# Performance work log

Hardware: AMD Instinct MI355X
Metric: run time of the kernel (lower is better)

## Reference

```python
import jax, jax.numpy as jnp
import numpy as np

B = 32768
MARGIN = 0.1
P = 2.0          # norm_degree
EPS_BN = 1e-3    # BatchNorm1d eps=0.001
EPS_PD = 1e-6    # F.pairwise_distance eps


def setup_inputs() -> dict:
    key = jax.random.key(0)
    ks = jax.random.split(key, 40)
    W = lambda k, o, i: jax.random.normal(k, (o, i), jnp.float32) * 0.01
    inp = {
        'img_p': jax.random.normal(ks[0], (B, 300), jnp.float32),
        'img_n': jax.random.normal(ks[1], (B, 300), jnp.float32),
        'tag':   jax.random.normal(ks[2], (B, 300), jnp.float32),
        'lat':   jax.random.uniform(ks[3], (B, 1), jnp.float32),
        'lon':   jax.random.uniform(ks[4], (B, 1), jnp.float32),
        # fc_i_1 (Linear 300->1024 + BN)
        'Wi1': W(ks[5], 1024, 300), 'bi1': jnp.zeros(1024), 'gi1': jnp.ones(1024), 'bti1': jnp.zeros(1024),
        # fc_i_2, fc_i_3
        'Wi2': W(ks[6], 1024, 1024), 'bi2': jnp.zeros(1024),
        'Wi3': W(ks[7], 300, 1024), 'bi3': jnp.zeros(300),
        # fc_loc (Linear 2->10 + BN)
        'Wloc': W(ks[8], 10, 2), 'bloc': jnp.zeros(10), 'gloc': jnp.ones(10), 'btloc': jnp.zeros(10),
        # fc_mm_1..3 (Linear + BN), fc_mm_4
        'Wm1': W(ks[9], 1024, 310), 'bm1': jnp.zeros(1024), 'gm1': jnp.ones(1024), 'btm1': jnp.zeros(1024),
        'Wm2': W(ks[10], 1024, 1024), 'bm2': jnp.zeros(1024), 'gm2': jnp.ones(1024), 'btm2': jnp.zeros(1024),
        'Wm3': W(ks[11], 1024, 1024), 'bm3': jnp.zeros(1024), 'gm3': jnp.ones(1024), 'btm3': jnp.zeros(1024),
        'Wm4': W(ks[12], 300, 1024), 'bm4': jnp.zeros(300),
    }
    return inp


def _fc_bn_relu(x, W, b, g, beta):
    # Linear -> BatchNorm1d (training mode, biased batch stats) -> ReLU
    y = x @ W.T + b
    m = jnp.mean(y, axis=0)
    v = jnp.mean((y - m) ** 2, axis=0)
    return jax.nn.relu((y - m) * jax.lax.rsqrt(v + EPS_BN) * g + beta)


def _pairwise_distance(x, y):
    # torch F.pairwise_distance with eps=1e-6
    return jnp.sum(jnp.abs(x - y + EPS_PD) ** P, axis=1) ** (1.0 / P)


def reference(img_p, img_n, tag, lat, lon,
              Wi1, bi1, gi1, bti1, Wi2, bi2, Wi3, bi3,
              Wloc, bloc, gloc, btloc,
              Wm1, bm1, gm1, btm1, Wm2, bm2, gm2, btm2,
              Wm3, bm3, gm3, btm3, Wm4, bm4):
    def img_branch(x):
        x = _fc_bn_relu(x, Wi1, bi1, gi1, bti1)
        x = x @ Wi2.T + bi2
        x = x @ Wi3.T + bi3
        return x
    p = img_branch(img_p)   # [B, 300]
    n = img_branch(img_n)   # [B, 300] (separate BN batch stats, as in torch)
    loc = jnp.concatenate([lat, lon], axis=1)           # [B, 2]
    loc = _fc_bn_relu(loc, Wloc, bloc, gloc, btloc)     # [B, 10]
    a = jnp.concatenate([loc, tag], axis=1)             # [B, 310]
    a = _fc_bn_relu(a, Wm1, bm1, gm1, btm1)
    a = _fc_bn_relu(a, Wm2, bm2, gm2, btm2)
    a = _fc_bn_relu(a, Wm3, bm3, gm3, btm3)
    a = a @ Wm4.T + bm4                                 # [B, 300]
    d_tp = _pairwise_distance(a, p)
    d_tn = _pairwise_distance(a, n)
    # vectorized replacement for the per-element python count loop
    correct = jnp.sum(d_tn - d_tp > MARGIN).astype(jnp.int32).reshape(1)
    return (p, n, a, correct)
```

## Files before the change

### kernel.cpp

```cpp
#include <hip/hip_runtime.h>

typedef _Float16 f16;
typedef _Float16 half8 __attribute__((ext_vector_type(8)));
typedef float f32x4 __attribute__((ext_vector_type(4)));

__device__ __forceinline__ void gl_lds16(const void* g, void* l) {
  __builtin_amdgcn_global_load_lds(
      (__attribute__((address_space(1))) void*)(size_t)g,
      (__attribute__((address_space(3))) void*)l, 16, 0, 0);
}

template <int EPI, int BNA>
__global__ __launch_bounds__(512, 2) void gemm256_k(
    const f16* __restrict__ A, int Ksteps, int KP,
    void* __restrict__ outp, int ldOut, int Ncols,
    float2* __restrict__ partial, int r1, int kz, int oz,
    const f16* __restrict__ B0, const float* __restrict__ bias0,
    const f16* __restrict__ sc0, const f16* __restrict__ sh0,
    const f16* __restrict__ B1, const float* __restrict__ bias1,
    const f16* __restrict__ sc1, const f16* __restrict__ sh1) {
  __shared__ char smem[135168];

  const int t = threadIdx.x;
  const int lane = t & 63;
  const int wave = t >> 6;
  const int wm = wave >> 2, wn = wave & 3;
  const int l16 = lane & 15, lg = lane >> 4;

  int bx = blockIdx.x, by = blockIdx.y;
  {
    const int nwg = gridDim.x * gridDim.y;
    const int wg = bx + gridDim.x * by;
    const int cpx = nwg >> 3;
    const int newid = (wg & 7) * cpx + (wg >> 3);
    bx = newid % gridDim.x;
    by = newid / gridDim.x;
  }
  const int m0 = by * 256;
  const int n0 = bx * 256;

  const f16* Bw = (by >= r1) ? B1 : B0;
  const float* bias = (by >= r1) ? bias1 : bias0;
  const f16* scH = (by >= r1) ? sc1 : sc0;
  const f16* shH = (by >= r1) ? sh1 : sh0;

  f32x4 acc[8][4] = {};

  const int rA = t >> 2;
  const int g16 = ((t & 3) ^ ((t >> 3) & 3)) * 16;
  const f16* Ap = A + (size_t)(m0 >> 8) * 256 * KP + (size_t)blockIdx.z * kz;
  const f16* Bp = Bw + (size_t)(n0 >> 8) * 256 * KP + (size_t)blockIdx.z * kz;
  const char* gA = (const char*)Ap + rA * 64 + g16;
  const char* gB = (const char*)Bp + rA * 64 + g16;

  auto stage = [&](int slot, int kt) {
    const char* pA = gA + (size_t)kt * 16384;
    const char* pB = gB + (size_t)kt * 16384;
    char* d = smem + slot * 32768 + t * 16;
    gl_lds16(pA, d);
    gl_lds16(pA + 8192, d + 8192);
    gl_lds16(pB, d + 16384);
    gl_lds16(pB + 8192, d + 24576);
  };

  if constexpr (BNA) {
    if (t < 128)
      gl_lds16((const char*)scH + t * 16, smem + 131072 + t * 16);
    else if (t < 256)
      gl_lds16((const char*)shH + (t - 128) * 16, smem + 133120 + (t - 128) * 16);
  }
  stage(0, 0);
  stage(1, 1);
  stage(2, 2);
  asm volatile("s_waitcnt vmcnt(8)" ::: "memory");
  __builtin_amdgcn_s_barrier();
  asm volatile("" ::: "memory");

  const int xsw = (lg ^ ((l16 >> 1) & 3)) << 4;
  const int oA0 = (wm * 128 + l16) * 64 + xsw;
  const int oB0 = (wn * 64 + l16) * 64 + xsw;

  for (int kt = 0; kt < Ksteps; ++kt) {
    const char* bufA = smem + (kt & 3) * 32768;
    const char* bufB = bufA + 16384;
    half8 af[8], bf0, bf1, scv, shv;
#pragma unroll
    for (int m = 0; m < 8; ++m) af[m] = *(const half8*)(bufA + oA0 + m * 1024);
    bf0 = *(const half8*)(bufB + oB0);
    bf1 = *(const half8*)(bufB + oB0 + 1024);
    if constexpr (BNA) {
      scv = *(const half8*)(smem + 131072 + kt * 64 + lg * 16);
      shv = *(const half8*)(smem + 133120 + kt * 64 + lg * 16);
    }
    if (kt + 3 < Ksteps) {
      const char* pA = gA + (size_t)(kt + 3) * 16384;
      char* d = smem + ((kt + 3) & 3) * 32768 + t * 16;
      gl_lds16(pA, d);
      gl_lds16(pA + 8192, d + 8192);
    }
    asm volatile("" ::: "memory");
    __builtin_amdgcn_s_barrier();
    asm volatile("s_waitcnt lgkmcnt(0)" ::: "memory");
    if constexpr (BNA) {
      const half8 zeroh = {};
#pragma unroll
      for (int m = 0; m < 8; ++m)
        af[m] = __builtin_elementwise_max((half8)(af[m] * scv + shv), zeroh);
    }
    __builtin_amdgcn_s_setprio(1);
#pragma unroll
    for (int m = 0; m < 8; ++m) {
      acc[m][0] = __builtin_amdgcn_mfma_f32_16x16x32_f16(af[m], bf0, acc[m][0], 0, 0, 0);
      acc[m][1] = __builtin_amdgcn_mfma_f32_16x16x32_f16(af[m], bf1, acc[m][1], 0, 0, 0);
    }
    __builtin_amdgcn_s_setprio(0);
    half8 bf2 = *(const half8*)(bufB + oB0 + 2048);
    half8 bf3 = *(const half8*)(bufB + oB0 + 3072);
    if (kt + 3 < Ksteps) {
      const char* pB = gB + (size_t)(kt + 3) * 16384;
      char* d = smem + ((kt + 3) & 3) * 32768 + t * 16;
      gl_lds16(pB, d + 16384);
      gl_lds16(pB + 8192, d + 24576);
      asm volatile("s_waitcnt vmcnt(8)" ::: "memory");
    } else if (kt == Ksteps - 3) {
      asm volatile("s_waitcnt vmcnt(4)" ::: "memory");
    } else if (kt == Ksteps - 2) {
      asm volatile("s_waitcnt vmcnt(0)" ::: "memory");
    }
    asm volatile("" ::: "memory");
    __builtin_amdgcn_s_barrier();
    asm volatile("s_waitcnt lgkmcnt(0)" ::: "memory");
    __builtin_amdgcn_s_setprio(1);
#pragma unroll
    for (int m = 0; m < 8; ++m) {
      acc[m][2] = __builtin_amdgcn_mfma_f32_16x16x32_f16(af[m], bf2, acc[m][2], 0, 0, 0);
      acc[m][3] = __builtin_amdgcn_mfma_f32_16x16x32_f16(af[m], bf3, acc[m][3], 0, 0, 0);
    }
    __builtin_amdgcn_s_setprio(0);
  }

  __syncthreads();

  float* const swv = (float*)smem + wave * 1152;
  float biasv[4];
#pragma unroll
  for (int n = 0; n < 4; ++n) {
    const int c = n0 + wn * 64 + n * 16 + l16;
    biasv[n] = (bias != nullptr && c < Ncols) ? bias[c] : 0.f;
  }
  float cs[4] = {}, cq[4] = {};
  const int rowr = lane >> 2;
  const int colc = (lane & 3) << 4;

#pragma unroll
  for (int m = 0; m < 8; ++m) {
#pragma unroll
    for (int n = 0; n < 4; ++n)
#pragma unroll
      for (int r = 0; r < 4; ++r) {
        const float v = acc[m][n][r] + biasv[n];
        swv[(lg * 4 + r) * 68 + n * 16 + l16] = v;
        if constexpr (EPI == 0) {
          cs[n] += v;
          cq[n] += v * v;
        }
      }
    asm volatile("s_waitcnt lgkmcnt(0)" ::: "memory");
    const float* sp = swv + rowr * 68 + colc;
    const int grow = m0 + wm * 128 + m * 16 + rowr;
    if constexpr (EPI == 2) {
      float* rp = (float*)outp + (size_t)blockIdx.z * oz + (size_t)grow * ldOut;
#pragma unroll
      for (int j = 0; j < 4; ++j) {
        const int c = n0 + wn * 64 + colc + j * 4;
        const f32x4 v = *(const f32x4*)(sp + j * 4);
        if (c + 3 < Ncols) {
          *(f32x4*)(rp + c) = v;
        } else {
#pragma unroll
          for (int e = 0; e < 4; ++e)
            if (c + e < Ncols) rp[c + e] = v[e];
        }
      }
    } else {
      const f32x4 v0 = *(const f32x4*)(sp);
      const f32x4 v1 = *(const f32x4*)(sp + 4);
      const f32x4 v2 = *(const f32x4*)(sp + 8);
      const f32x4 v3 = *(const f32x4*)(sp + 12);
      half8 h0, h1;
#pragma unroll
      for (int e = 0; e < 4; ++e) {
        h0[e] = (f16)v0[e];
        h0[4 + e] = (f16)v1[e];
        h1[e] = (f16)v2[e];
        h1[4 + e] = (f16)v3[e];
      }
      f16* o16 = (f16*)outp;
      const size_t dstE = (size_t)(grow >> 8) * 262144 +
                          (size_t)((n0 >> 5) + wn * 2 + (colc >> 5)) * 8192 +
                          (size_t)(grow & 255) * 32 + (colc & 31);
      *(half8*)(o16 + dstE) = h0;
      *(half8*)(o16 + dstE + 8) = h1;
    }
    asm volatile("s_waitcnt lgkmcnt(0)" ::: "memory");
  }

  if constexpr (EPI == 0) {
    float2* pp = partial + ((size_t)(by * 2 + wm) * 4 + lg) * 1024 + n0 + wn * 64 + l16;
#pragma unroll
    for (int n = 0; n < 4; ++n) pp[n * 16] = make_float2(cs[n], cq[n]);
  }
}

__global__ void bn_red_k(const float2* __restrict__ partial, float2* __restrict__ part2) {
  const int c = blockIdx.x * 256 + threadIdx.x;
  const int chunk = blockIdx.y;
  const float2* p = partial + (size_t)chunk * 64 * 1024 + c;
  float s = 0.f, q = 0.f;
#pragma unroll 4
  for (int i = 0; i < 64; ++i) {
    float2 v = p[(size_t)i * 1024];
    s += v.x;
    q += v.y;
  }
  part2[(size_t)chunk * 1024 + c] = make_float2(s, q);
}

__global__ void bn_fin_k(const float2* __restrict__ part2, int chunkStart, int nchunks,
                         const float* __restrict__ g, const float* __restrict__ beta,
                         f16* __restrict__ scH, f16* __restrict__ shH, float invB) {
  const int c = blockIdx.x * 256 + threadIdx.x;
  float s = 0.f, q = 0.f;
  const float2* p = part2 + (size_t)chunkStart * 1024 + c;
  for (int i = 0; i < nchunks; ++i) {
    float2 v = p[(size_t)i * 1024];
    s += v.x;
    q += v.y;
  }
  float m = s * invB;
  float var = q * invB - m * m;
  float sc = rsqrtf(var + 1e-3f) * g[c];
  scH[c] = (f16)sc;
  shH[c] = (f16)(beta[c] - m * sc);
}

__global__ void bn_fin3_k(const float2* __restrict__ part2, int cps, float invB,
                          const float* __restrict__ g0, const float* __restrict__ b0,
                          f16* __restrict__ so0, f16* __restrict__ sh0,
                          const float* __restrict__ g1, const float* __restrict__ b1,
                          f16* __restrict__ so1, f16* __restrict__ sh1,
                          const float* __restrict__ g2, const float* __restrict__ b2,
                          f16* __restrict__ so2, f16* __restrict__ sh2) {
  const int j = blockIdx.y;
  const float* g = j == 0 ? g0 : (j == 1 ? g1 : g2);
  const float* bt = j == 0 ? b0 : (j == 1 ? b1 : b2);
  f16* so = j == 0 ? so0 : (j == 1 ? so1 : so2);
  f16* sh = j == 0 ? sh0 : (j == 1 ? sh1 : sh2);
  const int c = blockIdx.x * 256 + threadIdx.x;
  float s = 0.f, q = 0.f;
  const float2* p = part2 + (size_t)j * cps * 1024 + c;
  for (int i = 0; i < cps; ++i) {
    float2 v = p[(size_t)i * 1024];
    s += v.x;
    q += v.y;
  }
  float m = s * invB;
  float var = q * invB - m * m;
  float sc = rsqrtf(var + 1e-3f) * g[c];
  so[c] = (f16)sc;
  sh[c] = (f16)(bt[c] - m * sc);
}

__global__ void cvt_all_k(const float* __restrict__ Wi1, const float* __restrict__ Wm1,
                          const float* __restrict__ Wi3, const float* __restrict__ Wm2,
                          const float* __restrict__ Wm3, const float* __restrict__ Wm4,
                          f16* __restrict__ Wi1p, f16* __restrict__ Wm1p,
                          f16* __restrict__ Wi3p, f16* __restrict__ Wm2p,
                          f16* __restrict__ Wm3p, f16* __restrict__ Wm4p) {
  const int k = blockIdx.x * 256 + threadIdx.x;
  const int row = blockIdx.y;
  const float* src;
  f16* dst;
  int n, K, KP, Nreal;
  if (row < 2048) {
    KP = 384;
    if (row < 1024) { src = Wi1; dst = Wi1p; n = row; K = 300; Nreal = 1024; }
    else { src = Wm1; dst = Wm1p; n = row - 1024; K = 310; Nreal = 1024; }
  } else {
    KP = 1024;
    if (row < 2560) { src = Wi3; dst = Wi3p; n = row - 2048; K = 1024; Nreal = 300; }
    else if (row < 3584) { src = Wm2; dst = Wm2p; n = row - 2560; K = 1024; Nreal = 1024; }
    else if (row < 4608) { src = Wm3; dst = Wm3p; n = row - 3584; K = 1024; Nreal = 1024; }
    else { src = Wm4; dst = Wm4p; n = row - 4608; K = 1024; Nreal = 300; }
  }
  if (k >= KP) return;
  float v = (n < Nreal && k < K) ? src[(size_t)n * K + k] : 0.f;
  dst[(size_t)(n >> 8) * 256 * KP + (size_t)(k >> 5) * 8192 +
      (size_t)(n & 255) * 32 + (k & 31)] = (f16)v;
}

__global__ void cvt_wT_k(const float* __restrict__ W, f16* __restrict__ Wt) {
  __shared__ f16 tile[64][65];
  const int bx = blockIdx.x * 64, by = blockIdx.y * 64;
  const int tc = threadIdx.x & 63, tr = threadIdx.x >> 6;
#pragma unroll
  for (int r = tr; r < 64; r += 4)
    tile[r][tc] = (f16)W[(size_t)(by + r) * 1024 + bx + tc];
  __syncthreads();
#pragma unroll
  for (int r = tr; r < 64; r += 4) {
    const int nr = bx + r;
    const int kc = by + tc;
    Wt[(size_t)(nr >> 8) * 262144 + (size_t)(kc >> 5) * 8192 +
       (size_t)(nr & 255) * 32 + (kc & 31)] = tile[tc][r];
  }
}

__global__ void cvt_in_k(const float* __restrict__ ip, const float* __restrict__ in_,
                         const float* __restrict__ tg, f16* __restrict__ Ain, int B) {
  const int gid = blockIdx.x * 256 + threadIdx.x;
  const int row = gid / 48;
  const int c0 = (gid - row * 48) * 8;
  if (row >= B) return;
  half8 vp = {}, vn = {}, vm = {};
  const float* rp = ip + (size_t)row * 300;
  const float* rn = in_ + (size_t)row * 300;
  const float* rt = tg + (size_t)row * 300;
#pragma unroll
  for (int e = 0; e < 8; ++e) {
    const int c = c0 + e;
    if (c < 300) {
      vp[e] = (f16)rp[c];
      vn[e] = (f16)rn[c];
    }
    if (c >= 10 && c < 310) vm[e] = (f16)rt[c - 10];
  }
  const size_t o = (size_t)(row >> 8) * 98304 + (size_t)(c0 >> 5) * 8192 +
                   (size_t)(row & 255) * 32 + (c0 & 31);
  const size_t pstr = (size_t)(B >> 8) * 98304;
  *(half8*)(Ain + o) = vp;
  *(half8*)(Ain + pstr + o) = vn;
  *(half8*)(Ain + 2 * pstr + o) = vm;
}

__global__ void fold_red_k(const float* __restrict__ pf, f16* __restrict__ Wf) {
  const int i = blockIdx.x * 256 + threadIdx.x;
  float s = 0.f;
#pragma unroll
  for (int z = 0; z < 8; ++z) s += pf[(size_t)z * 524288 + i];
  const int n = i >> 10, k = i & 1023;
  Wf[(size_t)(n >> 8) * 262144 + (size_t)(k >> 5) * 8192 +
     (size_t)(n & 255) * 32 + (k & 31)] = (f16)s;
}

__global__ void bfold_k(const f16* __restrict__ Wi3p, const float* __restrict__ bi2,
                        const float* __restrict__ bi3, float* __restrict__ bf) {
  const int n = blockIdx.x;
  const int t = threadIdx.x;
  const size_t nb = (size_t)(n >> 8) * 262144 + (size_t)(n & 255) * 32;
  float s = 0.f;
  for (int j = t; j < 1024; j += 256)
    s += (float)Wi3p[nb + (size_t)(j >> 5) * 8192 + (j & 31)] * bi2[j];
#pragma unroll
  for (int off = 32; off; off >>= 1) s += __shfl_xor(s, off);
  __shared__ float red[4];
  if ((t & 63) == 0) red[t >> 6] = s;
  __syncthreads();
  if (t == 0) bf[n] = red[0] + red[1] + red[2] + red[3] + (n < 300 ? bi3[n] : 0.f);
}

__global__ void loc_stats_k(const float* __restrict__ lat, const float* __restrict__ lon,
                            const float* __restrict__ Wloc, const float* __restrict__ bloc,
                            float* __restrict__ partial) {
  const int t = threadIdx.x;
  const int row = blockIdx.x * 256 + t;
  float la = lat[row], lo = lon[row];
  float s[10], q[10];
#pragma unroll
  for (int j = 0; j < 10; ++j) {
    float y = la * Wloc[j * 2] + lo * Wloc[j * 2 + 1] + bloc[j];
    s[j] = y;
    q[j] = y * y;
  }
#pragma unroll
  for (int j = 0; j < 10; ++j)
    for (int off = 32; off; off >>= 1) {
      s[j] += __shfl_xor(s[j], off);
      q[j] += __shfl_xor(q[j], off);
    }
  __shared__ float red[4][20];
  const int wave = t >> 6, lane = t & 63;
  if (lane == 0) {
#pragma unroll
    for (int j = 0; j < 10; ++j) {
      red[wave][j] = s[j];
      red[wave][10 + j] = q[j];
    }
  }
  __syncthreads();
  if (t < 20) partial[blockIdx.x * 20 + t] = red[0][t] + red[1][t] + red[2][t] + red[3][t];
}

__global__ void loc_fin_k(const float* __restrict__ partial, int nblk,
                          const float* __restrict__ g, const float* __restrict__ beta,
                          float2* __restrict__ ss, float invB) {
  int t = threadIdx.x;
  if (t < 10) {
    float s = 0.f, q = 0.f;
    for (int b = 0; b < nblk; ++b) {
      s += partial[b * 20 + t];
      q += partial[b * 20 + 10 + t];
    }
    float m = s * invB;
    float var = q * invB - m * m;
    float sc = rsqrtf(var + 1e-3f) * g[t];
    ss[t] = make_float2(sc, beta[t] - m * sc);
  }
}

__global__ void loc_write_k(const float* __restrict__ lat, const float* __restrict__ lon,
                            const float* __restrict__ Wloc, const float* __restrict__ bloc,
                            const float2* __restrict__ ss, f16* __restrict__ Am) {
  const int row = blockIdx.x * 256 + threadIdx.x;
  float la = lat[row], lo = lon[row];
  f16* dst = Am + (size_t)(row >> 8) * 98304 + (size_t)(row & 255) * 32;
#pragma unroll
  for (int j = 0; j < 10; ++j) {
    float y = la * Wloc[j * 2] + lo * Wloc[j * 2 + 1] + bloc[j];
    float2 sv = ss[j];
    dst[j] = (f16)fmaxf(y * sv.x + sv.y, 0.f);
  }
}

__global__ void count_k(const float* __restrict__ P, const float* __restrict__ Nn,
                        const float* __restrict__ Aa, int B, int* __restrict__ cnt) {
  const int gw = (blockIdx.x * blockDim.x + threadIdx.x) >> 6;
  const int lane = threadIdx.x & 63;
  const int nw = (gridDim.x * blockDim.x) >> 6;
  int local = 0;
  for (int row = gw; row < B; row += nw) {
    const float* ar = Aa + (size_t)row * 300;
    const float* pr = P + (size_t)row * 300;
    const float* nr = Nn + (size_t)row * 300;
    float sp = 0.f, sn = 0.f;
    for (int e = lane; e < 300; e += 64) {
      float av = ar[e];
      float d1 = av - pr[e] + 1e-6f;
      float d2 = av - nr[e] + 1e-6f;
      sp += d1 * d1;
      sn += d2 * d2;
    }
#pragma unroll
    for (int off = 32; off; off >>= 1) {
      sp += __shfl_xor(sp, off);
      sn += __shfl_xor(sn, off);
    }
    if (lane == 0 && (sqrtf(sn) - sqrtf(sp) > 0.1f)) ++local;
  }
  if (lane == 0 && local) atomicAdd(cnt, local);
}

__global__ void zero_i32(int* p) {
  if (threadIdx.x == 0 && blockIdx.x == 0) *p = 0;
}
__global__ void write_cnt_k(const int* c, float* o) {
  if (threadIdx.x == 0 && blockIdx.x == 0) *o = (float)(*c);
}

extern "C" void kernel_launch(void* const* d_in, const int* in_sizes, int n_in,
                              void* d_out, int out_size, void* d_ws, size_t ws_size,
                              hipStream_t stream) {
  const float* img_p = (const float*)d_in[0];
  const float* img_n = (const float*)d_in[1];
  const float* tag = (const float*)d_in[2];
  const float* lat = (const float*)d_in[3];
  const float* lon = (const float*)d_in[4];
  const float* Wi1 = (const float*)d_in[5];
  const float* bi1 = (const float*)d_in[6];
  const float* gi1 = (const float*)d_in[7];
  const float* bti1 = (const float*)d_in[8];
  const float* Wi2 = (const float*)d_in[9];
  const float* bi2 = (const float*)d_in[10];
  const float* Wi3 = (const float*)d_in[11];
  const float* bi3 = (const float*)d_in[12];
  const float* Wloc = (const float*)d_in[13];
  const float* bloc = (const float*)d_in[14];
  const float* gloc = (const float*)d_in[15];
  const float* btloc = (const float*)d_in[16];
  const float* Wm1 = (const float*)d_in[17];
  const float* bm1 = (const float*)d_in[18];
  const float* gm1 = (const float*)d_in[19];
  const float* btm1 = (const float*)d_in[20];
  const float* Wm2 = (const float*)d_in[21];
  const float* bm2 = (const float*)d_in[22];
  const float* gm2 = (const float*)d_in[23];
  const float* btm2 = (const float*)d_in[24];
  const float* Wm3 = (const float*)d_in[25];
  const float* bm3 = (const float*)d_in[26];
  const float* gm3 = (const float*)d_in[27];
  const float* btm3 = (const float*)d_in[28];
  const float* Wm4 = (const float*)d_in[29];
  const float* bm4 = (const float*)d_in[30];

  const int B = in_sizes[3];
  const int MT = B / 256;
  float* out = (float*)d_out;
  float* outP = out;
  float* outN = out + (size_t)B * 300;
  float* outA = out + (size_t)2 * B * 300;
  float* outC = out + (size_t)3 * B * 300;

  char* w = (char*)d_ws;
  auto alloc = [&](size_t bytes) {
    char* p = w;
    w += (bytes + 255) & ~(size_t)255;
    return p;
  };

  f16* Wi1p = (f16*)alloc((size_t)1024 * 384 * 2);
  f16* Wm1p = (f16*)alloc((size_t)1024 * 384 * 2);
  f16* Wi2T = (f16*)alloc((size_t)1024 * 1024 * 2);
  f16* Wi3p = (f16*)alloc((size_t)512 * 1024 * 2);
  f16* Wm2p = (f16*)alloc((size_t)1024 * 1024 * 2);
  f16* Wm3p = (f16*)alloc((size_t)1024 * 1024 * 2);
  f16* Wm4p = (f16*)alloc((size_t)512 * 1024 * 2);
  f16* Wfold = (f16*)alloc((size_t)512 * 1024 * 2);
  float* bfold = (float*)alloc(512 * 4);
  f16* ssT = (f16*)alloc(10 * 1024 * 2);
  f16 *scP1 = ssT, *shP1 = ssT + 1024, *scN1 = ssT + 2048, *shN1 = ssT + 3072;
  f16 *scM1 = ssT + 4096, *shM1 = ssT + 5120, *scM2 = ssT + 6144, *shM2 = ssT + 7168;
  f16 *scM3 = ssT + 8192, *shM3 = ssT + 9216;
  float* locpart = (float*)alloc((size_t)(B / 256) * 20 * 4);
  float2* locss = (float2*)alloc(16 * 8);
  int* cnt = (int*)alloc(256);
  f16* Ain = (f16*)alloc((size_t)3 * B * 384 * 2);
  f16* Am = Ain + (size_t)2 * B * 384;
  f16* ACT0 = (f16*)alloc((size_t)3 * B * 1024 * 2);
  f16* ACT0m = ACT0 + (size_t)2 * B * 1024;
  f16* ACT1m = (f16*)alloc((size_t)B * 1024 * 2);
  float2* part = (float2*)alloc((size_t)3072 * 1024 * 8);
  float* partF = (float*)part;
  float2* part2 = (float2*)alloc((size_t)48 * 1024 * 8);
  (void)ws_size;
  (void)out_size;
  (void)n_in;

  const float invB = 1.f / (float)B;
  const int BIG = 1 << 30;

  cvt_all_k<<<dim3(4, 5120), 256, 0, stream>>>(Wi1, Wm1, Wi3, Wm2, Wm3, Wm4,
                                               Wi1p, Wm1p, Wi3p, Wm2p, Wm3p, Wm4p);
  cvt_wT_k<<<dim3(16, 16), 256, 0, stream>>>(Wi2, Wi2T);
  cvt_in_k<<<dim3(B * 48 / 256), 256, 0, stream>>>(img_p, img_n, tag, Ain, B);

  loc_stats_k<<<dim3(B / 256), 256, 0, stream>>>(lat, lon, Wloc, bloc, locpart);
  loc_fin_k<<<dim3(1), 64, 0, stream>>>(locpart, B / 256, gloc, btloc, locss, invB);
  loc_write_k<<<dim3(B / 256), 256, 0, stream>>>(lat, lon, Wloc, bloc, locss, Am);

  bfold_k<<<dim3(512), 256, 0, stream>>>(Wi3p, bi2, bi3, bfold);
  gemm256_k<2, 0><<<dim3(4, 2, 8), 512, 0, stream>>>(
      Wi3p, 4, 1024, partF, 1024, 1024, nullptr, BIG, 32768, 524288,
      Wi2T, nullptr, nullptr, nullptr, Wi2T, nullptr, nullptr, nullptr);
  fold_red_k<<<dim3(2048), 256, 0, stream>>>(partF, Wfold);

  gemm256_k<0, 0><<<dim3(4, 3 * MT), 512, 0, stream>>>(
      Ain, 12, 384, ACT0, 1024, 1024, part, 2 * MT, 0, 0,
      Wi1p, bi1, nullptr, nullptr, Wm1p, bm1, nullptr, nullptr);
  bn_red_k<<<dim3(4, 48), 256, 0, stream>>>(part, part2);
  bn_fin3_k<<<dim3(4, 3), 256, 0, stream>>>(
      part2, 16, invB,
      gi1, bti1, scP1, shP1, gi1, bti1, scN1, shN1, gm1, btm1, scM1, shM1);

  gemm256_k<2, 1><<<dim3(2, 2 * MT), 512, 0, stream>>>(
      ACT0, 32, 1024, outP, 300, 300, part, MT, 0, 0,
      Wfold, bfold, scP1, shP1, Wfold, bfold, scN1, shN1);

  gemm256_k<0, 1><<<dim3(4, MT), 512, 0, stream>>>(
      ACT0m, 32, 1024, ACT1m, 1024, 1024, part, BIG, 0, 0,
      Wm2p, bm2, scM1, shM1, Wm2p, bm2, scM1, shM1);
  bn_red_k<<<dim3(4, 16), 256, 0, stream>>>(part, part2);
  bn_fin_k<<<dim3(4), 256, 0, stream>>>(part2, 0, 16, gm2, btm2, scM2, shM2, invB);
  gemm256_k<0, 1><<<dim3(4, MT), 512, 0, stream>>>(
      ACT1m, 32, 1024, ACT0, 1024, 1024, part, BIG, 0, 0,
      Wm3p, bm3, scM2, shM2, Wm3p, bm3, scM2, shM2);
  bn_red_k<<<dim3(4, 16), 256, 0, stream>>>(part, part2);
  bn_fin_k<<<dim3(4), 256, 0, stream>>>(part2, 0, 16, gm3, btm3, scM3, shM3, invB);
  gemm256_k<2, 1><<<dim3(2, MT), 512, 0, stream>>>(
      ACT0, 32, 1024, outA, 300, 300, part, BIG, 0, 0,
      Wm4p, bm4, scM3, shM3, Wm4p, bm4, scM3, shM3);

  zero_i32<<<1, 64, 0, stream>>>(cnt);
  count_k<<<dim3(1024), 256, 0, stream>>>(outP, outN, outA, B, cnt);
  write_cnt_k<<<1, 64, 0, stream>>>(cnt, outC);
}
```

Baseline: 704.2 us.

## Shrink GEMM tile to 128x256 with 3-stage LDS pipeline for higher occupancy

Halves the M dimension of the GEMM block tile from 256 to 128 and moves from a 4-slot to a 3-slot LDS ring, which cuts shared memory from about 132KB to 76KB. Launch bounds are raised to allow more resident workgroups per CU, with the aim of hiding latency better. The BN partial-stat buffers and reduction grids are doubled to match the larger number of row tiles. In exchange, each block reuses its B operand half as much and does more global traffic per FLOP, and the prefetch distance drops from 3 to 2 stages.

```diff
diff --git a/kernel.cpp b/kernel.cpp
--- a/kernel.cpp
+++ b/kernel.cpp
@@ -11,7 +11,7 @@
 }
 
 template <int EPI, int BNA>
-__global__ __launch_bounds__(512, 2) void gemm256_k(
+__global__ __launch_bounds__(512, 4) void gemm128_k(
     const f16* __restrict__ A, int Ksteps, int KP,
     void* __restrict__ outp, int ldOut, int Ncols,
     float2* __restrict__ partial, int r1, int kz, int oz,
@@ -19,7 +19,7 @@
     const f16* __restrict__ sc0, const f16* __restrict__ sh0,
     const f16* __restrict__ B1, const float* __restrict__ bias1,
     const f16* __restrict__ sc1, const f16* __restrict__ sh1) {
-  __shared__ char smem[135168];
+  __shared__ char smem[77824];
 
   const int t = threadIdx.x;
   const int lane = t & 63;
@@ -36,7 +36,7 @@
     bx = newid % gridDim.x;
     by = newid / gridDim.x;
   }
-  const int m0 = by * 256;
+  const int m0 = by * 128;
   const int n0 = bx * 256;
 
   const f16* Bw = (by >= r1) ? B1 : B0;
@@ -44,86 +44,79 @@
   const f16* scH = (by >= r1) ? sc1 : sc0;
   const f16* shH = (by >= r1) ? sh1 : sh0;
 
-  f32x4 acc[8][4] = {};
+  f32x4 acc[4][4] = {};
 
   const int rA = t >> 2;
   const int g16 = ((t & 3) ^ ((t >> 3) & 3)) * 16;
-  const f16* Ap = A + (size_t)(m0 >> 8) * 256 * KP + (size_t)blockIdx.z * kz;
-  const f16* Bp = Bw + (size_t)(n0 >> 8) * 256 * KP + (size_t)blockIdx.z * kz;
-  const char* gA = (const char*)Ap + rA * 64 + g16;
-  const char* gB = (const char*)Bp + rA * 64 + g16;
-
-  auto stage = [&](int slot, int kt) {
-    const char* pA = gA + (size_t)kt * 16384;
-    const char* pB = gB + (size_t)kt * 16384;
-    char* d = smem + slot * 32768 + t * 16;
-    gl_lds16(pA, d);
-    gl_lds16(pA + 8192, d + 8192);
-    gl_lds16(pB, d + 16384);
-    gl_lds16(pB + 8192, d + 24576);
+  const f16* Apan = A + (size_t)(m0 >> 8) * 256 * KP + (size_t)blockIdx.z * kz;
+  const f16* Bpan = Bw + (size_t)(n0 >> 8) * 256 * KP + (size_t)blockIdx.z * kz;
+  const char* gA = (const char*)Apan + (m0 & 255) * 64 + rA * 64 + g16;
+  const char* gB = (const char*)Bpan + rA * 64 + g16;
+
+  auto stageA = [&](int slot, int kt) {
+    gl_lds16(gA + (size_t)kt * 16384, smem + slot * 24576 + t * 16);
+  };
+  auto stageB = [&](int slot, int kt) {
+    const char* p = gB + (size_t)kt * 16384;
+    char* d = smem + slot * 24576 + 8192 + t * 16;
+    gl_lds16(p, d);
+    gl_lds16(p + 8192, d + 8192);
   };
 
   if constexpr (BNA) {
     if (t < 128)
-      gl_lds16((const char*)scH + t * 16, smem + 131072 + t * 16);
+      gl_lds16((const char*)scH + t * 16, smem + 73728 + t * 16);
     else if (t < 256)
-      gl_lds16((const char*)shH + (t - 128) * 16, smem + 133120 + (t - 128) * 16);
-  }
-  stage(0, 0);
-  stage(1, 1);
-  stage(2, 2);
-  asm volatile("s_waitcnt vmcnt(8)" ::: "memory");
+      gl_lds16((const char*)shH + (t - 128) * 16, smem + 75776 + (t - 128) * 16);
+  }
+  stageA(0, 0);
+  stageB(0, 0);
+  stageA(1, 1);
+  stageB(1, 1);
+  stageA(2, 2);
+  stageB(2, 2);
+  asm volatile("s_waitcnt vmcnt(6)" ::: "memory");
   __builtin_amdgcn_s_barrier();
   asm volatile("" ::: "memory");
 
   const int xsw = (lg ^ ((l16 >> 1) & 3)) << 4;
-  const int oA0 = (wm * 128 + l16) * 64 + xsw;
-  const int oB0 = (wn * 64 + l16) * 64 + xsw;
+  const int oA0 = (wm * 64 + l16) * 64 + xsw;
+  const int oB0 = 8192 + (wn * 64 + l16) * 64 + xsw;
 
   for (int kt = 0; kt < Ksteps; ++kt) {
-    const char* bufA = smem + (kt & 3) * 32768;
-    const char* bufB = bufA + 16384;
-    half8 af[8], bf0, bf1, scv, shv;
-#pragma unroll
-    for (int m = 0; m < 8; ++m) af[m] = *(const half8*)(bufA + oA0 + m * 1024);
-    bf0 = *(const half8*)(bufB + oB0);
-    bf1 = *(const half8*)(bufB + oB0 + 1024);
+    const int slot = kt % 3;
+    const char* buf = smem + slot * 24576;
+    half8 af[4], bf0, bf1, scv, shv;
+#pragma unroll
+    for (int m = 0; m < 4; ++m) af[m] = *(const half8*)(buf + oA0 + m * 1024);
+    bf0 = *(const half8*)(buf + oB0);
+    bf1 = *(const half8*)(buf + oB0 + 1024);
     if constexpr (BNA) {
-      scv = *(const half8*)(smem + 131072 + kt * 64 + lg * 16);
-      shv = *(const half8*)(smem + 133120 + kt * 64 + lg * 16);
-    }
-    if (kt + 3 < Ksteps) {
-      const char* pA = gA + (size_t)(kt + 3) * 16384;
-      char* d = smem + ((kt + 3) & 3) * 32768 + t * 16;
-      gl_lds16(pA, d);
-      gl_lds16(pA + 8192, d + 8192);
-    }
+      scv = *(const half8*)(smem + 73728 + kt * 64 + lg * 16);
+      shv = *(const half8*)(smem + 75776 + kt * 64 + lg * 16);
+    }
+    if (kt + 2 < Ksteps) stageA((kt + 2) % 3, kt + 2);
     asm volatile("" ::: "memory");
     __builtin_amdgcn_s_barrier();
     asm volatile("s_waitcnt lgkmcnt(0)" ::: "memory");
     if constexpr (BNA) {
       const half8 zeroh = {};
 #pragma unroll
-      for (int m = 0; m < 8; ++m)
+      for (int m = 0; m < 4; ++m)
         af[m] = __builtin_elementwise_max((half8)(af[m] * scv + shv), zeroh);
     }
     __builtin_amdgcn_s_setprio(1);
 #pragma unroll
-    for (int m = 0; m < 8; ++m) {
+    for (int m = 0; m < 4; ++m) {
       acc[m][0] = __builtin_amdgcn_mfma_f32_16x16x32_f16(af[m], bf0, acc[m][0], 0, 0, 0);
       acc[m][1] = __builtin_amdgcn_mfma_f32_16x16x32_f16(af[m], bf1, acc[m][1], 0, 0, 0);
     }
     __builtin_amdgcn_s_setprio(0);
-    half8 bf2 = *(const half8*)(bufB + oB0 + 2048);
-    half8 bf3 = *(const half8*)(bufB + oB0 + 3072);
-    if (kt + 3 < Ksteps) {
-      const char* pB = gB + (size_t)(kt + 3) * 16384;
-      char* d = smem + ((kt + 3) & 3) * 32768 + t * 16;
-      gl_lds16(pB, d + 16384);
-      gl_lds16(pB + 8192, d + 24576);
-      asm volatile("s_waitcnt vmcnt(8)" ::: "memory");
-    } else if (kt == Ksteps - 3) {
-      asm volatile("s_waitcnt vmcnt(4)" ::: "memory");
+    half8 bf2 = *(const half8*)(buf + oB0 + 2048);
+    half8 bf3 = *(const half8*)(buf + oB0 + 3072);
+    if (kt + 2 < Ksteps) {
+      stageB((kt + 2) % 3, kt + 2);
+      asm volatile("s_waitcnt vmcnt(3)" ::: "memory");
     } else if (kt == Ksteps - 2) {
       asm volatile("s_waitcnt vmcnt(0)" ::: "memory");
     }
@@ -132,7 +125,7 @@
     asm volatile("s_waitcnt lgkmcnt(0)" ::: "memory");
     __builtin_amdgcn_s_setprio(1);
 #pragma unroll
-    for (int m = 0; m < 8; ++m) {
+    for (int m = 0; m < 4; ++m) {
       acc[m][2] = __builtin_amdgcn_mfma_f32_16x16x32_f16(af[m], bf2, acc[m][2], 0, 0, 0);
       acc[m][3] = __builtin_amdgcn_mfma_f32_16x16x32_f16(af[m], bf3, acc[m][3], 0, 0, 0);
     }
@@ -153,7 +146,7 @@
   const int colc = (lane & 3) << 4;
 
 #pragma unroll
-  for (int m = 0; m < 8; ++m) {
+  for (int m = 0; m < 4; ++m) {
 #pragma unroll
     for (int n = 0; n < 4; ++n)
 #pragma unroll
@@ -167,7 +160,7 @@
       }
     asm volatile("s_waitcnt lgkmcnt(0)" ::: "memory");
     const float* sp = swv + rowr * 68 + colc;
-    const int grow = m0 + wm * 128 + m * 16 + rowr;
+    const int grow = m0 + wm * 64 + m * 16 + rowr;
     if constexpr (EPI == 2) {
       float* rp = (float*)outp + (size_t)blockIdx.z * oz + (size_t)grow * ldOut;
 #pragma unroll
@@ -503,7 +496,7 @@
   const float* bm4 = (const float*)d_in[30];
 
   const int B = in_sizes[3];
-  const int MT = B / 256;
+  const int MT = B / 128;
   float* out = (float*)d_out;
   float* outP = out;
   float* outN = out + (size_t)B * 300;
@@ -538,9 +531,9 @@
   f16* ACT0 = (f16*)alloc((size_t)3 * B * 1024 * 2);
   f16* ACT0m = ACT0 + (size_t)2 * B * 1024;
   f16* ACT1m = (f16*)alloc((size_t)B * 1024 * 2);
-  float2* part = (float2*)alloc((size_t)3072 * 1024 * 8);
+  float2* part = (float2*)alloc((size_t)6144 * 1024 * 8);
   float* partF = (float*)part;
-  float2* part2 = (float2*)alloc((size_t)48 * 1024 * 8);
+  float2* part2 = (float2*)alloc((size_t)96 * 1024 * 8);
   (void)ws_size;
   (void)out_size;
   (void)n_in;
@@ -558,34 +551,34 @@
   loc_write_k<<<dim3(B / 256), 256, 0, stream>>>(lat, lon, Wloc, bloc, locss, Am);
 
   bfold_k<<<dim3(512), 256, 0, stream>>>(Wi3p, bi2, bi3, bfold);
-  gemm256_k<2, 0><<<dim3(4, 2, 8), 512, 0, stream>>>(
+  gemm128_k<2, 0><<<dim3(4, 4, 8), 512, 0, stream>>>(
       Wi3p, 4, 1024, partF, 1024, 1024, nullptr, BIG, 32768, 524288,
       Wi2T, nullptr, nullptr, nullptr, Wi2T, nullptr, nullptr, nullptr);
   fold_red_k<<<dim3(2048), 256, 0, stream>>>(partF, Wfold);
 
-  gemm256_k<0, 0><<<dim3(4, 3 * MT), 512, 0, stream>>>(
+  gemm128_k<0, 0><<<dim3(4, 3 * MT), 512, 0, stream>>>(
       Ain, 12, 384, ACT0, 1024, 1024, part, 2 * MT, 0, 0,
       Wi1p, bi1, nullptr, nullptr, Wm1p, bm1, nullptr, nullptr);
-  bn_red_k<<<dim3(4, 48), 256, 0, stream>>>(part, part2);
+  bn_red_k<<<dim3(4, 96), 256, 0, stream>>>(part, part2);
   bn_fin3_k<<<dim3(4, 3), 256, 0, stream>>>(
-      part2, 16, invB,
+      part2, 32, invB,
       gi1, bti1, scP1, shP1, gi1, bti1, scN1, shN1, gm1, btm1, scM1, shM1);
 
-  gemm256_k<2, 1><<<dim3(2, 2 * MT), 512, 0, stream>>>(
+  gemm128_k<2, 1><<<dim3(2, 2 * MT), 512, 0, stream>>>(
       ACT0, 32, 1024, outP, 300, 300, part, MT, 0, 0,
       Wfold, bfold, scP1, shP1, Wfold, bfold, scN1, shN1);
 
-  gemm256_k<0, 1><<<dim3(4, MT), 512, 0, stream>>>(
+  gemm128_k<0, 1><<<dim3(4, MT), 512, 0, stream>>>(
       ACT0m, 32, 1024, ACT1m, 1024, 1024, part, BIG, 0, 0,
       Wm2p, bm2, scM1, shM1, Wm2p, bm2, scM1, shM1);
-  bn_red_k<<<dim3(4, 16), 256, 0, stream>>>(part, part2);
-  bn_fin_k<<<dim3(4), 256, 0, stream>>>(part2, 0, 16, gm2, btm2, scM2, shM2, invB);
-  gemm256_k<0, 1><<<dim3(4, MT), 512, 0, stream>>>(
+  bn_red_k<<<dim3(4, 32), 256, 0, stream>>>(part, part2);
+  bn_fin_k<<<dim3(4), 256, 0, stream>>>(part2, 0, 32, gm2, btm2, scM2, shM2, invB);
+  gemm128_k<0, 1><<<dim3(4, MT), 512, 0, stream>>>(
       ACT1m, 32, 1024, ACT0, 1024, 1024, part, BIG, 0, 0,
       Wm3p, bm3, scM2, shM2, Wm3p, bm3, scM2, shM2);
-  bn_red_k<<<dim3(4, 16), 256, 0, stream>>>(part, part2);
-  bn_fin_k<<<dim3(4), 256, 0, stream>>>(part2, 0, 16, gm3, btm3, scM3, shM3, invB);
-  gemm256_k<2, 1><<<dim3(2, MT), 512, 0, stream>>>(
+  bn_red_k<<<dim3(4, 32), 256, 0, stream>>>(part, part2);
+  bn_fin_k<<<dim3(4), 256, 0, stream>>>(part2, 0, 32, gm3, btm3, scM3, shM3, invB);
+  gemm128_k<2, 1><<<dim3(2, MT), 512, 0, stream>>>(
       ACT0, 32, 1024, outA, 300, 300, part, BIG, 0, 0,
       Wm4p, bm4, scM3, shM3, Wm4p, bm4, scM3, shM3);
 
```

After: 719.9 us. 2.2% more time.
